# Kernel optimization log

Measured on AMD Instinct MI355X. Metric: run time of the kernel, lower is better.

## Reference

```python
import jax, jax.numpy as jnp
import numpy as np

B = 1024        # probe batch
Q = 65536       # queue_size (number of identities in momentum queue)
D = 512         # feat_dim
MARGIN = 0.4
SCALE = 32.0
HARD_NEG = 10   # min(max(int(Q*0.0002), 3), 10)


def setup_inputs() -> dict:
    key = jax.random.key(0)
    k1, k2, k3, k4 = jax.random.split(key, 4)
    p = jax.random.normal(k1, (B, D), dtype=jnp.float32)
    p = p / jnp.linalg.norm(p, axis=1, keepdims=True)
    queue = jax.random.uniform(k2, (2, Q, D), dtype=jnp.float32)
    queue = queue / jnp.linalg.norm(queue, axis=2, keepdims=True)  # F.normalize(queue, dim=2)
    label = jax.random.randint(k3, (B,), 0, Q)
    label = jnp.where(jnp.arange(B) % 4 == 0, -1, label)
    # binary mask buffer marking queue slots whose second copy is active
    mask = (jax.random.uniform(k4, (Q, 1)) < 0.1).astype(jnp.float32)
    return {"p": p, "queue": queue, "mask": mask, "label": label}


def _add_margin_am(cos_theta, label):
    # cos_theta: [B, Q], label: [B] with -1 marking outliers
    pos_mask = label != -1                                  # [B]
    safe_label = jnp.where(pos_mask, label, 0)
    onehot = jax.nn.one_hot(safe_label, cos_theta.shape[1], dtype=cos_theta.dtype)
    # AM-softmax: subtract margin at the ground-truth logit, then scale + CE
    logits = (cos_theta - MARGIN * onehot) * SCALE          # [B, Q]
    log_z = jax.nn.logsumexp(logits, axis=1)                # [B]
    gt = jnp.take_along_axis(cos_theta, safe_label[:, None], axis=1)[:, 0]
    ce = log_z - (gt - MARGIN) * SCALE                      # per-row cross entropy
    n_pos = jnp.sum(pos_mask)
    cls_loss = jnp.where(
        n_pos > 0,
        jnp.sum(jnp.where(pos_mask, ce, 0.0)) / jnp.maximum(n_pos, 1),
        0.0,
    )
    # hard-negative mining over outlier rows: top-k (replaces torch argsort+gather)
    top_vals, _ = jax.lax.top_k(cos_theta, HARD_NEG)        # [B, HARD_NEG]
    hard = jnp.clip(top_vals, 0.0)
    neg_per_row = jnp.mean(hard, axis=1)                    # [B]
    n_neg = jnp.sum(~pos_mask)
    neg_loss = jnp.where(
        n_neg > 0,
        jnp.sum(jnp.where(~pos_mask, neg_per_row, 0.0)) / jnp.maximum(n_neg, 1),
        0.0,
    )
    return cls_loss + neg_loss


def reference(p, queue, mask, label):
    # cos_theta1 = F.linear(p, queue[0])
    cos1 = jnp.einsum('bd,qd->bq', p, queue[0])
    # weight = mask * queue[1] + (1 - mask) * queue[0]  (computed under no_grad in torch)
    weight = mask * queue[1] + (1.0 - mask) * queue[0]
    cos2 = jnp.einsum('bd,qd->bq', p, weight)
    loss = _add_margin_am(cos1, label) + _add_margin_am(cos2, label)
    return loss
```

## Files before the change

### kernel.cpp

```cpp
#include <hip/hip_runtime.h>
#include <stdint.h>

#define B_ 1024
#define Q_ 65536
#define D_ 512
#define MT 128
#define NT 128
#define BK 64
#define NSPLIT 64
#define NCHUNK (Q_ / NSPLIT)
#define NTILES (NCHUNK / NT)
#define KITERS (D_ / BK)

#define SCALE32 32.0f
#define C32 46.16624130844683f

#define WS_ACC  0
#define WS_LSE  4096
#define WS_TOPK (1u * 1024u * 1024u)
#define WS_PBF  (8u * 1024u * 1024u)
#define WS_QBF0 (12u * 1024u * 1024u)
#define WS_WBF  (76u * 1024u * 1024u)

#define SA_OFF 0
#define SB0_OFF 16384
#define SB1_OFF 32768

typedef __attribute__((ext_vector_type(8))) short short8;
typedef __attribute__((ext_vector_type(4))) short short4v;
typedef __attribute__((ext_vector_type(4))) float f32x4;

__device__ __forceinline__ unsigned short f2bf(float x) {
  union { float f; uint32_t u; } v; v.f = x;
  uint32_t r = v.u + 0x7fffu + ((v.u >> 16) & 1u);
  return (unsigned short)(r >> 16);
}

__device__ __forceinline__ float bf2f(short u) {
  union { uint32_t i; float f; } v;
  v.i = ((uint32_t)(unsigned short)u) << 16;
  return v.f;
}

__device__ __forceinline__ void async16(void* lds, const void* g) {
  void* gg = (void*)g;
  __builtin_amdgcn_global_load_lds(
      (__attribute__((address_space(1))) unsigned int*)gg,
      (__attribute__((address_space(3))) unsigned int*)lds,
      16, 0, 0);
}

__device__ __forceinline__ void tkins(float v,
    float& t0, float& t1, float& t2, float& t3, float& t4,
    float& t5, float& t6, float& t7, float& t8, float& t9) {
  if (v > t9) {
    t9 = (v > t8) ? t8 : v;
    t8 = (v > t8) ? ((v > t7) ? t7 : v) : t8;
    t7 = (v > t7) ? ((v > t6) ? t6 : v) : t7;
    t6 = (v > t6) ? ((v > t5) ? t5 : v) : t6;
    t5 = (v > t5) ? ((v > t4) ? t4 : v) : t5;
    t4 = (v > t4) ? ((v > t3) ? t3 : v) : t4;
    t3 = (v > t3) ? ((v > t2) ? t2 : v) : t3;
    t2 = (v > t2) ? ((v > t1) ? t1 : v) : t2;
    t1 = (v > t1) ? ((v > t0) ? t0 : v) : t1;
    t0 = (v > t0) ? v : t0;
  }
}

#define TKA(v, a) tkins((v), a[0], a[1], a[2], a[3], a[4], a[5], a[6], a[7], a[8], a[9])

__global__ void cvt_all(const float* __restrict__ q, const float* __restrict__ p,
                        const float* __restrict__ mask,
                        unsigned short* __restrict__ qbf0,
                        unsigned short* __restrict__ wbf,
                        unsigned short* __restrict__ pbf) {
  const int wv = threadIdx.x >> 6;
  const int lane = threadIdx.x & 63;
  const int b = blockIdx.x;
  if (b < Q_ / 4) {
    const int row = b * 4 + wv;
    const float* q0r = q + (size_t)row * D_ + lane * 8;
    float4 a = ((const float4*)q0r)[0];
    float4 bb = ((const float4*)q0r)[1];
    short8 o;
    o[0] = (short)f2bf(a.x); o[1] = (short)f2bf(a.y);
    o[2] = (short)f2bf(a.z); o[3] = (short)f2bf(a.w);
    o[4] = (short)f2bf(bb.x); o[5] = (short)f2bf(bb.y);
    o[6] = (short)f2bf(bb.z); o[7] = (short)f2bf(bb.w);
    *(short8*)(qbf0 + (size_t)row * D_ + lane * 8) = o;
    float m = mask[row];
    if (m != 0.0f) {
      const float* q1r = q0r + (size_t)Q_ * D_;
      float4 c = ((const float4*)q1r)[0];
      float4 d = ((const float4*)q1r)[1];
      a.x = fmaf(m, c.x - a.x, a.x); a.y = fmaf(m, c.y - a.y, a.y);
      a.z = fmaf(m, c.z - a.z, a.z); a.w = fmaf(m, c.w - a.w, a.w);
      bb.x = fmaf(m, d.x - bb.x, bb.x); bb.y = fmaf(m, d.y - bb.y, bb.y);
      bb.z = fmaf(m, d.z - bb.z, bb.z); bb.w = fmaf(m, d.w - bb.w, bb.w);
      o[0] = (short)f2bf(a.x); o[1] = (short)f2bf(a.y);
      o[2] = (short)f2bf(a.z); o[3] = (short)f2bf(a.w);
      o[4] = (short)f2bf(bb.x); o[5] = (short)f2bf(bb.y);
      o[6] = (short)f2bf(bb.z); o[7] = (short)f2bf(bb.w);
      *(short8*)(wbf + (size_t)row * D_ + lane * 8) = o;
    }
  } else {
    const int row = (b - Q_ / 4) * 4 + wv;
    const float* pr = p + (size_t)row * D_ + lane * 8;
    float4 a = ((const float4*)pr)[0];
    float4 bb = ((const float4*)pr)[1];
    short8 o;
    o[0] = (short)f2bf(a.x); o[1] = (short)f2bf(a.y);
    o[2] = (short)f2bf(a.z); o[3] = (short)f2bf(a.w);
    o[4] = (short)f2bf(bb.x); o[5] = (short)f2bf(bb.y);
    o[6] = (short)f2bf(bb.z); o[7] = (short)f2bf(bb.w);
    *(short8*)(pbf + (size_t)row * D_ + lane * 8) = o;
  }
}

__global__ __launch_bounds__(256, 2) void fused_gemm_partial(
    const unsigned short* __restrict__ pbf,
    const unsigned short* __restrict__ qbf0,
    const unsigned short* __restrict__ wbf,
    const float* __restrict__ maskp,
    const int* __restrict__ label,
    char* __restrict__ ws) {
  __shared__ __align__(16) unsigned char smem[49152];
  __shared__ float maskb[NT];
  __shared__ float zacc[MT][4];
  __shared__ int olist[MT];
  __shared__ int rowmap[MT];
  __shared__ int sh_ocount;

  const int tid = threadIdx.x;
  const int split = blockIdx.x;
  const int mblk = blockIdx.y;
  const int lane = tid & 63;
  const int wv = tid >> 6;
  const int wr = wv >> 1;
  const int wc = wv & 1;
  const int lr = lane & 15;
  const int lg = lane >> 4;

  if (tid == 0) sh_ocount = 0;
  if (tid < MT) {
    rowmap[tid] = -1;
    zacc[tid][0] = 0.0f; zacc[tid][1] = 0.0f;
    zacc[tid][2] = 0.0f; zacc[tid][3] = 0.0f;
  }
  __syncthreads();
  if (tid < MT) {
    if (label[mblk * MT + tid] == -1) {
      int k = atomicAdd(&sh_ocount, 1);
      olist[k] = tid;
    }
  }
  __syncthreads();
  const int noc = sh_ocount;
  if (tid < noc) rowmap[olist[tid]] = tid;
  __syncthreads();
  const int nchunks = (noc + 31) >> 5;

  const int srow = lane >> 3;
  const int sc16 = (lane & 7) ^ srow;
  const size_t g_lane_off = (size_t)srow * D_ + sc16 * 8;

  float T[10];
#pragma unroll
  for (int i = 0; i < 10; ++i) T[i] = -1e30f;

  for (int nt = 0; nt < NTILES; ++nt) {
    const int nbase = split * NCHUNK + nt * NT;
    if (tid < NT) maskb[tid] = maskp[nbase + tid];
    __syncthreads();

    const unsigned short* b1b[4];
#pragma unroll
    for (int t = 0; t < 4; ++t) {
      const int rowl = (wv * 4 + t) * 8 + srow;
      b1b[t] = (maskb[rowl] != 0.0f) ? wbf : qbf0;
    }

    f32x4 acc0[4][4], acc1[4][4];
#pragma unroll
    for (int i = 0; i < 4; ++i)
#pragma unroll
      for (int j = 0; j < 4; ++j) {
        f32x4 z = {0.0f, 0.0f, 0.0f, 0.0f};
        acc0[i][j] = z;
        acc1[i][j] = z;
      }

    for (int kk = 0; kk < KITERS; ++kk) {
      const size_t kcol = (size_t)kk * BK;
#pragma unroll
      for (int t = 0; t < 4; ++t) {
        const int slot = wv * 4 + t;
        const size_t rbase = (size_t)slot * 8;
        async16(smem + SA_OFF + slot * 1024,
                pbf + ((size_t)mblk * MT + rbase) * D_ + kcol + g_lane_off);
        async16(smem + SB0_OFF + slot * 1024,
                qbf0 + ((size_t)nbase + rbase) * D_ + kcol + g_lane_off);
        async16(smem + SB1_OFF + slot * 1024,
                b1b[t] + ((size_t)nbase + rbase) * D_ + kcol + g_lane_off);
      }
      __syncthreads();

#pragma unroll
      for (int s = 0; s < 2; ++s) {
        const int xs = ((s * 4 + lg) ^ (lr & 7)) * 16;
        short8 af[4], bf[4];
#pragma unroll
        for (int i = 0; i < 4; ++i)
          af[i] = *(const short8*)(smem + SA_OFF + (wr * 64 + i * 16 + lr) * 128 + xs);
#pragma unroll
        for (int j = 0; j < 4; ++j)
          bf[j] = *(const short8*)(smem + SB0_OFF + (wc * 64 + j * 16 + lr) * 128 + xs);
#pragma unroll
        for (int i = 0; i < 4; ++i)
#pragma unroll
          for (int j = 0; j < 4; ++j)
            acc0[i][j] = __builtin_amdgcn_mfma_f32_16x16x32_bf16(af[i], bf[j], acc0[i][j], 0, 0, 0);
#pragma unroll
        for (int j = 0; j < 4; ++j)
          bf[j] = *(const short8*)(smem + SB1_OFF + (wc * 64 + j * 16 + lr) * 128 + xs);
#pragma unroll
        for (int i = 0; i < 4; ++i)
#pragma unroll
          for (int j = 0; j < 4; ++j)
            acc1[i][j] = __builtin_amdgcn_mfma_f32_16x16x32_bf16(af[i], bf[j], acc1[i][j], 0, 0, 0);
      }
      __syncthreads();
    }

#pragma unroll
    for (int i = 0; i < 4; ++i)
#pragma unroll
      for (int k = 0; k < 4; ++k) {
        float a0 = 0.0f, a1 = 0.0f;
#pragma unroll
        for (int j = 0; j < 4; ++j) {
          a0 += __builtin_amdgcn_exp2f(fmaf(acc0[i][j][k], C32, -C32));
          a1 += __builtin_amdgcn_exp2f(fmaf(acc1[i][j][k], C32, -C32));
        }
#pragma unroll
        for (int m = 1; m < 16; m <<= 1) {
          a0 += __shfl_xor(a0, m, 64);
          a1 += __shfl_xor(a1, m, 64);
        }
        if (lr == 0) {
          const int r = wr * 64 + i * 16 + lg * 4 + k;
          zacc[r][wc * 2 + 0] += a0;
          zacc[r][wc * 2 + 1] += a1;
        }
      }

    for (int c = 0; c < nchunks; ++c) {
      unsigned short* cp = (unsigned short*)smem;
#pragma unroll
      for (int i = 0; i < 4; ++i)
#pragma unroll
        for (int k = 0; k < 4; ++k) {
          const int r = wr * 64 + i * 16 + lg * 4 + k;
          const int o = rowmap[r];
          const int ol = o - c * 32;
          if (o >= 0 && ol >= 0 && ol < 32) {
#pragma unroll
            for (int j = 0; j < 4; ++j) {
              const int col = wc * 64 + j * 16 + lr;
              cp[ol * 128 + col] = f2bf(acc0[i][j][k]);
              cp[(32 + ol) * 128 + col] = f2bf(acc1[i][j][k]);
            }
          }
        }
      __syncthreads();

      {
        float tl[10];
#pragma unroll
        for (int r = 0; r < 10; ++r) tl[r] = -1e30f;
        const int pair = tid >> 2;
        const int q4 = tid & 3;
        const int orow = pair >> 1, mat = pair & 1;
        const int o = c * 32 + orow;
        if (o < noc) {
          const unsigned short* rp = cp + (mat * 32 + orow) * 128 + q4 * 32;
#pragma unroll
          for (int cc = 0; cc < 8; ++cc) {
            short4v v = *(const short4v*)(rp + cc * 4);
            TKA(bf2f(v.x), tl); TKA(bf2f(v.y), tl);
            TKA(bf2f(v.z), tl); TKA(bf2f(v.w), tl);
          }
          float ot[10];
#pragma unroll
          for (int r = 0; r < 10; ++r) ot[r] = __shfl_xor(tl[r], 1, 64);
#pragma unroll
          for (int r = 0; r < 10; ++r) TKA(ot[r], tl);
#pragma unroll
          for (int r = 0; r < 10; ++r) ot[r] = __shfl_xor(tl[r], 2, 64);
#pragma unroll
          for (int r = 0; r < 10; ++r) TKA(ot[r], tl);
          if (q4 == 0) {
            if (c == 0) {
#pragma unroll
              for (int r = 0; r < 10; ++r) TKA(tl[r], T);
            } else {
              float* slot = (float*)(ws + WS_TOPK) +
                  ((size_t)(mat * B_ + mblk * MT + olist[o]) * NSPLIT + split) * 10;
              if (nt == 0) {
#pragma unroll
                for (int r = 0; r < 10; ++r) slot[r] = tl[r];
              } else {
                float cur[10];
#pragma unroll
                for (int r = 0; r < 10; ++r) cur[r] = slot[r];
#pragma unroll
                for (int r = 0; r < 10; ++r) TKA(tl[r], cur);
#pragma unroll
                for (int r = 0; r < 10; ++r) slot[r] = cur[r];
              }
            }
          }
        }
      }
      __syncthreads();
    }
  }

  if (tid < MT) {
    float2* lseo = (float2*)(ws + WS_LSE);
    lseo[(size_t)(mblk * MT + tid) * NSPLIT + split] =
        make_float2(zacc[tid][0] + zacc[tid][2], zacc[tid][1] + zacc[tid][3]);
  }
  {
    const int pair = tid >> 2;
    const int q4 = tid & 3;
    const int orow = pair >> 1, mat = pair & 1;
    if (q4 == 0 && orow < noc && orow < 32) {
      float* slot = (float*)(ws + WS_TOPK) +
          ((size_t)(mat * B_ + mblk * MT + olist[orow]) * NSPLIT + split) * 10;
#pragma unroll
      for (int r = 0; r < 10; ++r) slot[r] = T[r];
    }
  }
}

__global__ void finalize_rows(
    const float* __restrict__ p, const float* __restrict__ queue,
    const float* __restrict__ maskp, const int* __restrict__ label,
    char* __restrict__ ws, float* __restrict__ out) {
  const int row = blockIdx.x;
  const int l = threadIdx.x >> 6;
  const int lane = threadIdx.x & 63;
  const int lab = label[row];
  float* wsf = (float*)ws;
  int* wsi = (int*)ws;

  if (lab != -1) {
    const float2* lsep = (const float2*)(ws + WS_LSE) + (size_t)row * NSPLIT;
    float2 zz = lsep[lane];
    float z = (l == 0) ? zz.x : zz.y;
#pragma unroll
    for (int o = 1; o < 64; o <<= 1) z += __shfl_xor(z, o, 64);

    const float* prow = p + (size_t)row * D_;
    const float* q0r = queue + (size_t)lab * D_;
    const float* q1r = queue + ((size_t)Q_ + (size_t)lab) * D_;
    int c = lane * 8;
    float4 a0 = *(const float4*)(prow + c);
    float4 a1 = *(const float4*)(prow + c + 4);
    float4 b0 = *(const float4*)(q0r + c);
    float4 b1 = *(const float4*)(q0r + c + 4);
    float d0 = a0.x * b0.x + a0.y * b0.y + a0.z * b0.z + a0.w * b0.w
             + a1.x * b1.x + a1.y * b1.y + a1.z * b1.z + a1.w * b1.w;
    float d1 = 0.0f;
    if (l == 1) {
      float4 c0 = *(const float4*)(q1r + c);
      float4 c1 = *(const float4*)(q1r + c + 4);
      d1 = a0.x * c0.x + a0.y * c0.y + a0.z * c0.z + a0.w * c0.w
         + a1.x * c1.x + a1.y * c1.y + a1.z * c1.z + a1.w * c1.w;
    }
#pragma unroll
    for (int o = 1; o < 64; o <<= 1) {
      d0 += __shfl_xor(d0, o, 64);
      d1 += __shfl_xor(d1, o, 64);
    }
    float gt;
    if (l == 0) gt = d0;
    else { float m = maskp[lab]; gt = fmaf(m, d1 - d0, d0); }

    if (lane == 0) {
      float e1 = __builtin_amdgcn_exp2f(fmaf(gt, C32, -C32));
      float e2 = __builtin_amdgcn_exp2f(fmaf(gt - 0.4f, C32, -C32));
      float Zc = z - e1 + e2;
      float ce = 32.0f + __logf(Zc) - (gt - 0.4f) * SCALE32;
      atomicAdd(&wsf[0], ce);
      if (l == 0) atomicAdd(&wsi[2], 1);
    }
  } else {
    const float* tp = (const float*)(ws + WS_TOPK) +
                      ((size_t)l * B_ + row) * NSPLIT * 10 + (size_t)lane * 10;
    float t0 = tp[0], t1 = tp[1], t2 = tp[2], t3 = tp[3], t4 = tp[4];
    float t5 = tp[5], t6 = tp[6], t7 = tp[7], t8 = tp[8], t9 = tp[9];
    float ssum = 0.0f;
#pragma unroll
    for (int r10 = 0; r10 < 10; ++r10) {
      float v = t0;
      int idx = lane;
#pragma unroll
      for (int o = 1; o < 64; o <<= 1) {
        float ov = __shfl_xor(v, o, 64);
        int oi = __shfl_xor(idx, o, 64);
        bool take = (ov > v) || (ov == v && oi < idx);
        v = take ? ov : v;
        idx = take ? oi : idx;
      }
      ssum += fmaxf(v, 0.0f);
      if (idx == lane) {
        t0 = t1; t1 = t2; t2 = t3; t3 = t4; t4 = t5;
        t5 = t6; t6 = t7; t7 = t8; t8 = t9; t9 = -1e30f;
      }
    }
    if (lane == 0) {
      atomicAdd(&wsf[1], ssum * 0.1f);
      if (l == 0) atomicAdd(&wsi[3], 1);
    }
  }

  __syncthreads();
  if (threadIdx.x == 0) {
    __threadfence();
    int old = atomicAdd(&wsi[4], 1);
    if (old == B_ - 1) {
      float ce = atomicAdd(&wsf[0], 0.0f);
      float ng = atomicAdd(&wsf[1], 0.0f);
      int np = atomicAdd(&wsi[2], 0);
      int nn = atomicAdd(&wsi[3], 0);
      float loss = 0.0f;
      if (np > 0) loss += ce / (float)np;
      if (nn > 0) loss += ng / (float)nn;
      out[0] = loss;
    }
  }
}

extern "C" void kernel_launch(void* const* d_in, const int* in_sizes, int n_in,
                              void* d_out, int out_size, void* d_ws, size_t ws_size,
                              hipStream_t stream) {
  const float* p     = (const float*)d_in[0];
  const float* queue = (const float*)d_in[1];
  const float* maskp = (const float*)d_in[2];
  const int*   label = (const int*)d_in[3];
  float* out = (float*)d_out;
  char* ws = (char*)d_ws;

  unsigned short* pbf  = (unsigned short*)(ws + WS_PBF);
  unsigned short* qbf0 = (unsigned short*)(ws + WS_QBF0);
  unsigned short* wbf  = (unsigned short*)(ws + WS_WBF);

  hipMemsetAsync(ws, 0, 32, stream);

  cvt_all<<<Q_ / 4 + B_ / 4, 256, 0, stream>>>(queue, p, maskp, qbf0, wbf, pbf);

  dim3 g1(NSPLIT, B_ / MT);
  fused_gemm_partial<<<g1, 256, 0, stream>>>(pbf, qbf0, wbf, maskp, label, ws);
  finalize_rows<<<B_, 128, 0, stream>>>(p, queue, maskp, label, ws, out);
}
```

Measured before the change: 598.0 us.

## Triple-buffer GEMM k-loop with async prefetch, widen to 8 waves, deterministic final reduce

The GEMM kernel moves from 256 to 512 threads (8 waves, each covering 32 columns) and replaces the load-sync-compute-sync k-loop with a 3-stage shared-memory ring. Global-to-LDS copies for k+2 are issued while k is computed, with vmcnt waits and one barrier per step. The end-of-loss atomics and the last-block counter are replaced by per-row writes plus a separate single-block reduce kernel, which removes the memset. LDS use grows to 144KB per block, which likely limits occupancy to one block per CU despite the launch bound.

Result: slower. 638.2 us (+6.7%).

```diff
diff --git a/kernel.cpp b/kernel.cpp
--- a/kernel.cpp
+++ b/kernel.cpp
@@ -15,13 +15,14 @@
 #define SCALE32 32.0f
 #define C32 46.16624130844683f
 
-#define WS_ACC  0
-#define WS_LSE  4096
+#define WS_ROWV 0
+#define WS_LSE  16384
 #define WS_TOPK (1u * 1024u * 1024u)
 #define WS_PBF  (8u * 1024u * 1024u)
 #define WS_QBF0 (12u * 1024u * 1024u)
 #define WS_WBF  (76u * 1024u * 1024u)
 
+#define SBUF 49152
 #define SA_OFF 0
 #define SB0_OFF 16384
 #define SB1_OFF 32768
@@ -117,16 +118,16 @@
   }
 }
 
-__global__ __launch_bounds__(256, 2) void fused_gemm_partial(
+__global__ __launch_bounds__(512, 2) void fused_gemm_partial(
     const unsigned short* __restrict__ pbf,
     const unsigned short* __restrict__ qbf0,
     const unsigned short* __restrict__ wbf,
     const float* __restrict__ maskp,
     const int* __restrict__ label,
     char* __restrict__ ws) {
-  __shared__ __align__(16) unsigned char smem[49152];
+  __shared__ __align__(16) unsigned char smem[3 * SBUF];
   __shared__ float maskb[NT];
-  __shared__ float zacc[MT][4];
+  __shared__ float zacc[MT][8];
   __shared__ int olist[MT];
   __shared__ int rowmap[MT];
   __shared__ int sh_ocount;
@@ -136,16 +137,16 @@
   const int mblk = blockIdx.y;
   const int lane = tid & 63;
   const int wv = tid >> 6;
-  const int wr = wv >> 1;
-  const int wc = wv & 1;
+  const int wr = wv >> 2;
+  const int wc = wv & 3;
   const int lr = lane & 15;
   const int lg = lane >> 4;
 
   if (tid == 0) sh_ocount = 0;
   if (tid < MT) {
     rowmap[tid] = -1;
-    zacc[tid][0] = 0.0f; zacc[tid][1] = 0.0f;
-    zacc[tid][2] = 0.0f; zacc[tid][3] = 0.0f;
+#pragma unroll
+    for (int c = 0; c < 8; ++c) zacc[tid][c] = 0.0f;
   }
   __syncthreads();
   if (tid < MT) {
@@ -173,63 +174,76 @@
     if (tid < NT) maskb[tid] = maskp[nbase + tid];
     __syncthreads();
 
-    const unsigned short* b1b[4];
-#pragma unroll
-    for (int t = 0; t < 4; ++t) {
-      const int rowl = (wv * 4 + t) * 8 + srow;
+    const unsigned short* b1b[2];
+#pragma unroll
+    for (int t = 0; t < 2; ++t) {
+      const int rowl = (wv * 2 + t) * 8 + srow;
       b1b[t] = (maskb[rowl] != 0.0f) ? wbf : qbf0;
     }
 
-    f32x4 acc0[4][4], acc1[4][4];
+    f32x4 acc0[4][2], acc1[4][2];
 #pragma unroll
     for (int i = 0; i < 4; ++i)
 #pragma unroll
-      for (int j = 0; j < 4; ++j) {
+      for (int j = 0; j < 2; ++j) {
         f32x4 z = {0.0f, 0.0f, 0.0f, 0.0f};
         acc0[i][j] = z;
         acc1[i][j] = z;
       }
 
+    auto stage = [&](int buf, int kk) {
+      const size_t kcol = (size_t)kk * BK;
+      unsigned char* sb = smem + (size_t)buf * SBUF;
+#pragma unroll
+      for (int t = 0; t < 2; ++t) {
+        const int slot = wv * 2 + t;
+        const size_t rbase = (size_t)slot * 8;
+        async16(sb + SA_OFF + slot * 1024,
+                pbf + ((size_t)mblk * MT + rbase) * D_ + kcol + g_lane_off);
+        async16(sb + SB0_OFF + slot * 1024,
+                qbf0 + ((size_t)nbase + rbase) * D_ + kcol + g_lane_off);
+        async16(sb + SB1_OFF + slot * 1024,
+                b1b[t] + ((size_t)nbase + rbase) * D_ + kcol + g_lane_off);
+      }
+    };
+
+    stage(0, 0);
+    stage(1, 1);
+
+#pragma unroll
     for (int kk = 0; kk < KITERS; ++kk) {
-      const size_t kcol = (size_t)kk * BK;
-#pragma unroll
-      for (int t = 0; t < 4; ++t) {
-        const int slot = wv * 4 + t;
-        const size_t rbase = (size_t)slot * 8;
-        async16(smem + SA_OFF + slot * 1024,
-                pbf + ((size_t)mblk * MT + rbase) * D_ + kcol + g_lane_off);
-        async16(smem + SB0_OFF + slot * 1024,
-                qbf0 + ((size_t)nbase + rbase) * D_ + kcol + g_lane_off);
-        async16(smem + SB1_OFF + slot * 1024,
-                b1b[t] + ((size_t)nbase + rbase) * D_ + kcol + g_lane_off);
-      }
-      __syncthreads();
-
+      if (kk < KITERS - 1)
+        asm volatile("s_waitcnt vmcnt(6)" ::: "memory");
+      else
+        asm volatile("s_waitcnt vmcnt(0)" ::: "memory");
+      __builtin_amdgcn_s_barrier();
+      if (kk < KITERS - 2) stage((kk + 2) % 3, kk + 2);
+
+      const unsigned char* sb = smem + (size_t)(kk % 3) * SBUF;
 #pragma unroll
       for (int s = 0; s < 2; ++s) {
         const int xs = ((s * 4 + lg) ^ (lr & 7)) * 16;
-        short8 af[4], bf[4];
+        short8 af[4], bf0[2], bf1[2];
 #pragma unroll
         for (int i = 0; i < 4; ++i)
-          af[i] = *(const short8*)(smem + SA_OFF + (wr * 64 + i * 16 + lr) * 128 + xs);
-#pragma unroll
-        for (int j = 0; j < 4; ++j)
-          bf[j] = *(const short8*)(smem + SB0_OFF + (wc * 64 + j * 16 + lr) * 128 + xs);
+          af[i] = *(const short8*)(sb + SA_OFF + (wr * 64 + i * 16 + lr) * 128 + xs);
+#pragma unroll
+        for (int j = 0; j < 2; ++j)
+          bf0[j] = *(const short8*)(sb + SB0_OFF + (wc * 32 + j * 16 + lr) * 128 + xs);
+#pragma unroll
+        for (int j = 0; j < 2; ++j)
+          bf1[j] = *(const short8*)(sb + SB1_OFF + (wc * 32 + j * 16 + lr) * 128 + xs);
 #pragma unroll
         for (int i = 0; i < 4; ++i)
 #pragma unroll
-          for (int j = 0; j < 4; ++j)
-            acc0[i][j] = __builtin_amdgcn_mfma_f32_16x16x32_bf16(af[i], bf[j], acc0[i][j], 0, 0, 0);
-#pragma unroll
-        for (int j = 0; j < 4; ++j)
-          bf[j] = *(const short8*)(smem + SB1_OFF + (wc * 64 + j * 16 + lr) * 128 + xs);
+          for (int j = 0; j < 2; ++j)
+            acc0[i][j] = __builtin_amdgcn_mfma_f32_16x16x32_bf16(af[i], bf0[j], acc0[i][j], 0, 0, 0);
 #pragma unroll
         for (int i = 0; i < 4; ++i)
 #pragma unroll
-          for (int j = 0; j < 4; ++j)
-            acc1[i][j] = __builtin_amdgcn_mfma_f32_16x16x32_bf16(af[i], bf[j], acc1[i][j], 0, 0, 0);
-      }
-      __syncthreads();
+          for (int j = 0; j < 2; ++j)
+            acc1[i][j] = __builtin_amdgcn_mfma_f32_16x16x32_bf16(af[i], bf1[j], acc1[i][j], 0, 0, 0);
+      }
     }
 
 #pragma unroll
@@ -238,7 +252,7 @@
       for (int k = 0; k < 4; ++k) {
         float a0 = 0.0f, a1 = 0.0f;
 #pragma unroll
-        for (int j = 0; j < 4; ++j) {
+        for (int j = 0; j < 2; ++j) {
           a0 += __builtin_amdgcn_exp2f(fmaf(acc0[i][j][k], C32, -C32));
           a1 += __builtin_amdgcn_exp2f(fmaf(acc1[i][j][k], C32, -C32));
         }
@@ -265,8 +279,8 @@
           const int ol = o - c * 32;
           if (o >= 0 && ol >= 0 && ol < 32) {
 #pragma unroll
-            for (int j = 0; j < 4; ++j) {
-              const int col = wc * 64 + j * 16 + lr;
+            for (int j = 0; j < 2; ++j) {
+              const int col = wc * 32 + j * 16 + lr;
               cp[ol * 128 + col] = f2bf(acc0[i][j][k]);
               cp[(32 + ol) * 128 + col] = f2bf(acc1[i][j][k]);
             }
@@ -282,7 +296,7 @@
         const int q4 = tid & 3;
         const int orow = pair >> 1, mat = pair & 1;
         const int o = c * 32 + orow;
-        if (o < noc) {
+        if (orow < 32 && o < noc) {
           const unsigned short* rp = cp + (mat * 32 + orow) * 128 + q4 * 32;
 #pragma unroll
           for (int cc = 0; cc < 8; ++cc) {
@@ -324,12 +338,15 @@
       }
       __syncthreads();
     }
-  }
-
+    if (nchunks > 1) asm volatile("s_waitcnt vmcnt(0)" ::: "memory");
+  }
+
+  __syncthreads();
   if (tid < MT) {
     float2* lseo = (float2*)(ws + WS_LSE);
-    lseo[(size_t)(mblk * MT + tid) * NSPLIT + split] =
-        make_float2(zacc[tid][0] + zacc[tid][2], zacc[tid][1] + zacc[tid][3]);
+    lseo[(size_t)(mblk * MT + tid) * NSPLIT + split] = make_float2(
+        zacc[tid][0] + zacc[tid][2] + zacc[tid][4] + zacc[tid][6],
+        zacc[tid][1] + zacc[tid][3] + zacc[tid][5] + zacc[tid][7]);
   }
   {
     const int pair = tid >> 2;
@@ -352,8 +369,7 @@
   const int l = threadIdx.x >> 6;
   const int lane = threadIdx.x & 63;
   const int lab = label[row];
-  float* wsf = (float*)ws;
-  int* wsi = (int*)ws;
+  float* rowv = (float*)(ws + WS_ROWV);
 
   if (lab != -1) {
     const float2* lsep = (const float2*)(ws + WS_LSE) + (size_t)row * NSPLIT;
@@ -393,8 +409,7 @@
       float e2 = __builtin_amdgcn_exp2f(fmaf(gt - 0.4f, C32, -C32));
       float Zc = z - e1 + e2;
       float ce = 32.0f + __logf(Zc) - (gt - 0.4f) * SCALE32;
-      atomicAdd(&wsf[0], ce);
-      if (l == 0) atomicAdd(&wsi[2], 1);
+      rowv[l * B_ + row] = ce;
     }
   } else {
     const float* tp = (const float*)(ws + WS_TOPK) +
@@ -420,26 +435,42 @@
         t5 = t6; t6 = t7; t7 = t8; t8 = t9; t9 = -1e30f;
       }
     }
-    if (lane == 0) {
-      atomicAdd(&wsf[1], ssum * 0.1f);
-      if (l == 0) atomicAdd(&wsi[3], 1);
-    }
-  }
-
+    if (lane == 0) rowv[l * B_ + row] = ssum * 0.1f;
+  }
+}
+
+__global__ void reduce_final(const int* __restrict__ label,
+                             const char* __restrict__ ws,
+                             float* __restrict__ out) {
+  __shared__ float sce[4], sng[4];
+  __shared__ int snp[4], snn[4];
+  const int tid = threadIdx.x;
+  const float* rowv = (const float*)(ws + WS_ROWV);
+  float ce = 0.0f, ng = 0.0f;
+  int np = 0, nn = 0;
+  for (int r = tid; r < B_; r += 256) {
+    float v = rowv[r] + rowv[B_ + r];
+    if (label[r] != -1) { ce += v; ++np; }
+    else { ng += v; ++nn; }
+  }
+#pragma unroll
+  for (int o = 1; o < 64; o <<= 1) {
+    ce += __shfl_xor(ce, o, 64);
+    ng += __shfl_xor(ng, o, 64);
+    np += __shfl_xor(np, o, 64);
+    nn += __shfl_xor(nn, o, 64);
+  }
+  const int wv = tid >> 6, lane = tid & 63;
+  if (lane == 0) { sce[wv] = ce; sng[wv] = ng; snp[wv] = np; snn[wv] = nn; }
   __syncthreads();
-  if (threadIdx.x == 0) {
-    __threadfence();
-    int old = atomicAdd(&wsi[4], 1);
-    if (old == B_ - 1) {
-      float ce = atomicAdd(&wsf[0], 0.0f);
-      float ng = atomicAdd(&wsf[1], 0.0f);
-      int np = atomicAdd(&wsi[2], 0);
-      int nn = atomicAdd(&wsi[3], 0);
-      float loss = 0.0f;
-      if (np > 0) loss += ce / (float)np;
-      if (nn > 0) loss += ng / (float)nn;
-      out[0] = loss;
-    }
+  if (tid == 0) {
+    float c = 0.0f, g = 0.0f; int p = 0, n = 0;
+#pragma unroll
+    for (int i = 0; i < 4; ++i) { c += sce[i]; g += sng[i]; p += snp[i]; n += snn[i]; }
+    float loss = 0.0f;
+    if (p > 0) loss += c / (float)p;
+    if (n > 0) loss += g / (float)n;
+    out[0] = loss;
   }
 }
 
@@ -457,11 +488,10 @@
   unsigned short* qbf0 = (unsigned short*)(ws + WS_QBF0);
   unsigned short* wbf  = (unsigned short*)(ws + WS_WBF);
 
-  hipMemsetAsync(ws, 0, 32, stream);
-
   cvt_all<<<Q_ / 4 + B_ / 4, 256, 0, stream>>>(queue, p, maskp, qbf0, wbf, pbf);
 
   dim3 g1(NSPLIT, B_ / MT);
-  fused_gemm_partial<<<g1, 256, 0, stream>>>(pbf, qbf0, wbf, maskp, label, ws);
+  fused_gemm_partial<<<g1, 512, 0, stream>>>(pbf, qbf0, wbf, maskp, label, ws);
   finalize_rows<<<B_, 128, 0, stream>>>(p, queue, maskp, label, ws, out);
-}
+  reduce_final<<<1, 256, 0, stream>>>(label, ws, out);
+}
```

## Compute second GEMM only on masked queue rows via compacted sparse correction

Applied to the files above, without the earlier changes.

Since weight equals queue[0] wherever mask is 0, the main GEMM now computes only p·queue[0]. A separate sparse GEMM runs over a compacted list of masked rows (built by a single-block scan) and adds the logsumexp correction and top-k candidates for cos2. This roughly halves MFMA work and B-operand traffic in the dense kernel, at the cost of a serial scan kernel, an extra gather GEMM launched over the maximum tile grid (most blocks exit early), and larger per-row merge work in finalize. The global atomics and last-block reduction are replaced by per-row outputs and a small final reduction kernel.

Result: slower. 689.9 us (+15.4%).

```diff
diff --git a/kernel.cpp b/kernel.cpp
--- a/kernel.cpp
+++ b/kernel.cpp
@@ -11,20 +11,21 @@
 #define NCHUNK (Q_ / NSPLIT)
 #define NTILES (NCHUNK / NT)
 #define KITERS (D_ / BK)
+#define MAXCT (Q_ / NT)
 
 #define SCALE32 32.0f
 #define C32 46.16624130844683f
 
-#define WS_ACC  0
-#define WS_LSE  4096
-#define WS_TOPK (1u * 1024u * 1024u)
-#define WS_PBF  (8u * 1024u * 1024u)
-#define WS_QBF0 (12u * 1024u * 1024u)
-#define WS_WBF  (76u * 1024u * 1024u)
-
-#define SA_OFF 0
-#define SB0_OFF 16384
-#define SB1_OFF 32768
+#define WS_ROWV  0u
+#define WS_META  16384u
+#define WS_MLIST 65536u
+#define WS_LSE   524288u
+#define WS_TOPK  (1u * 1024u * 1024u)
+#define WS_ZCORR (7u * 1024u * 1024u)
+#define WS_TOPKS (9u * 1024u * 1024u)
+#define WS_PBF   (30u * 1024u * 1024u)
+#define WS_QBF0  (32u * 1024u * 1024u)
+#define WS_WBF   (96u * 1024u * 1024u)
 
 typedef __attribute__((ext_vector_type(8))) short short8;
 typedef __attribute__((ext_vector_type(4))) short short4v;
@@ -68,6 +69,40 @@
 }
 
 #define TKA(v, a) tkins((v), a[0], a[1], a[2], a[3], a[4], a[5], a[6], a[7], a[8], a[9])
+
+__global__ __launch_bounds__(1024, 1) void compact_scan(
+    const float* __restrict__ mask, char* __restrict__ ws) {
+  __shared__ int wsum[16];
+  __shared__ int carry;
+  const int tid = threadIdx.x;
+  const int lane = tid & 63, wv = tid >> 6;
+  int* mlist = (int*)(ws + WS_MLIST);
+  if (tid == 0) carry = 0;
+  __syncthreads();
+  for (int c = 0; c < Q_ / 1024; ++c) {
+    const int r = c * 1024 + tid;
+    const bool m = mask[r] != 0.0f;
+    unsigned long long b = __ballot(m);
+    const int lpre = __popcll(b & ((1ull << lane) - 1ull));
+    if (lane == 0) wsum[wv] = __popcll(b);
+    __syncthreads();
+    int wbase = 0;
+#pragma unroll
+    for (int i = 0; i < 16; ++i) wbase += (i < wv) ? wsum[i] : 0;
+    int ctot = 0;
+#pragma unroll
+    for (int i = 0; i < 16; ++i) ctot += wsum[i];
+    if (m) mlist[carry + wbase + lpre] = r;
+    __syncthreads();
+    if (tid == 0) carry += ctot;
+    __syncthreads();
+  }
+  if (tid == 0) {
+    int* meta = (int*)(ws + WS_META);
+    meta[0] = carry;
+    meta[1] = (carry + NT - 1) / NT;
+  }
+}
 
 __global__ void cvt_all(const float* __restrict__ q, const float* __restrict__ p,
                         const float* __restrict__ mask,
@@ -120,13 +155,12 @@
 __global__ __launch_bounds__(256, 2) void fused_gemm_partial(
     const unsigned short* __restrict__ pbf,
     const unsigned short* __restrict__ qbf0,
-    const unsigned short* __restrict__ wbf,
     const float* __restrict__ maskp,
     const int* __restrict__ label,
     char* __restrict__ ws) {
-  __shared__ __align__(16) unsigned char smem[49152];
+  __shared__ __align__(16) unsigned char smem[32768];
   __shared__ float maskb[NT];
-  __shared__ float zacc[MT][4];
+  __shared__ float zacc[MT][2];
   __shared__ int olist[MT];
   __shared__ int rowmap[MT];
   __shared__ int sh_ocount;
@@ -142,11 +176,7 @@
   const int lg = lane >> 4;
 
   if (tid == 0) sh_ocount = 0;
-  if (tid < MT) {
-    rowmap[tid] = -1;
-    zacc[tid][0] = 0.0f; zacc[tid][1] = 0.0f;
-    zacc[tid][2] = 0.0f; zacc[tid][3] = 0.0f;
-  }
+  if (tid < MT) rowmap[tid] = -1;
   __syncthreads();
   if (tid < MT) {
     if (label[mblk * MT + tid] == -1) {
@@ -167,41 +197,42 @@
   float T[10];
 #pragma unroll
   for (int i = 0; i < 10; ++i) T[i] = -1e30f;
+  float zreg[4][4];
+#pragma unroll
+  for (int i = 0; i < 4; ++i)
+#pragma unroll
+    for (int k = 0; k < 4; ++k) zreg[i][k] = 0.0f;
 
   for (int nt = 0; nt < NTILES; ++nt) {
     const int nbase = split * NCHUNK + nt * NT;
     if (tid < NT) maskb[tid] = maskp[nbase + tid];
     __syncthreads();
 
-    const unsigned short* b1b[4];
-#pragma unroll
-    for (int t = 0; t < 4; ++t) {
-      const int rowl = (wv * 4 + t) * 8 + srow;
-      b1b[t] = (maskb[rowl] != 0.0f) ? wbf : qbf0;
-    }
-
-    f32x4 acc0[4][4], acc1[4][4];
+    f32x4 acc[4][4];
 #pragma unroll
     for (int i = 0; i < 4; ++i)
 #pragma unroll
       for (int j = 0; j < 4; ++j) {
         f32x4 z = {0.0f, 0.0f, 0.0f, 0.0f};
-        acc0[i][j] = z;
-        acc1[i][j] = z;
-      }
+        acc[i][j] = z;
+      }
+
+    const unsigned short* abase[4];
+    const unsigned short* bbase[4];
+#pragma unroll
+    for (int t = 0; t < 4; ++t) {
+      const int slot = wv * 4 + t;
+      abase[t] = pbf + ((size_t)mblk * MT + slot * 8) * D_ + g_lane_off;
+      bbase[t] = qbf0 + ((size_t)nbase + slot * 8) * D_ + g_lane_off;
+    }
 
     for (int kk = 0; kk < KITERS; ++kk) {
       const size_t kcol = (size_t)kk * BK;
 #pragma unroll
       for (int t = 0; t < 4; ++t) {
         const int slot = wv * 4 + t;
-        const size_t rbase = (size_t)slot * 8;
-        async16(smem + SA_OFF + slot * 1024,
-                pbf + ((size_t)mblk * MT + rbase) * D_ + kcol + g_lane_off);
-        async16(smem + SB0_OFF + slot * 1024,
-                qbf0 + ((size_t)nbase + rbase) * D_ + kcol + g_lane_off);
-        async16(smem + SB1_OFF + slot * 1024,
-                b1b[t] + ((size_t)nbase + rbase) * D_ + kcol + g_lane_off);
+        async16(smem + slot * 1024, abase[t] + kcol);
+        async16(smem + 16384 + slot * 1024, bbase[t] + kcol);
       }
       __syncthreads();
 
@@ -211,48 +242,33 @@
         short8 af[4], bf[4];
 #pragma unroll
         for (int i = 0; i < 4; ++i)
-          af[i] = *(const short8*)(smem + SA_OFF + (wr * 64 + i * 16 + lr) * 128 + xs);
+          af[i] = *(const short8*)(smem + (wr * 64 + i * 16 + lr) * 128 + xs);
 #pragma unroll
         for (int j = 0; j < 4; ++j)
-          bf[j] = *(const short8*)(smem + SB0_OFF + (wc * 64 + j * 16 + lr) * 128 + xs);
+          bf[j] = *(const short8*)(smem + 16384 + (wc * 64 + j * 16 + lr) * 128 + xs);
 #pragma unroll
         for (int i = 0; i < 4; ++i)
 #pragma unroll
           for (int j = 0; j < 4; ++j)
-            acc0[i][j] = __builtin_amdgcn_mfma_f32_16x16x32_bf16(af[i], bf[j], acc0[i][j], 0, 0, 0);
+            acc[i][j] = __builtin_amdgcn_mfma_f32_16x16x32_bf16(af[i], bf[j], acc[i][j], 0, 0, 0);
+      }
+      __syncthreads();
+    }
+
+#pragma unroll
+    for (int i = 0; i < 4; ++i)
+#pragma unroll
+      for (int k = 0; k < 4; ++k) {
+        float a0 = 0.0f;
 #pragma unroll
         for (int j = 0; j < 4; ++j)
-          bf[j] = *(const short8*)(smem + SB1_OFF + (wc * 64 + j * 16 + lr) * 128 + xs);
-#pragma unroll
-        for (int i = 0; i < 4; ++i)
-#pragma unroll
-          for (int j = 0; j < 4; ++j)
-            acc1[i][j] = __builtin_amdgcn_mfma_f32_16x16x32_bf16(af[i], bf[j], acc1[i][j], 0, 0, 0);
-      }
-      __syncthreads();
-    }
-
-#pragma unroll
-    for (int i = 0; i < 4; ++i)
-#pragma unroll
-      for (int k = 0; k < 4; ++k) {
-        float a0 = 0.0f, a1 = 0.0f;
-#pragma unroll
-        for (int j = 0; j < 4; ++j) {
-          a0 += __builtin_amdgcn_exp2f(fmaf(acc0[i][j][k], C32, -C32));
-          a1 += __builtin_amdgcn_exp2f(fmaf(acc1[i][j][k], C32, -C32));
-        }
-#pragma unroll
-        for (int m = 1; m < 16; m <<= 1) {
-          a0 += __shfl_xor(a0, m, 64);
-          a1 += __shfl_xor(a1, m, 64);
-        }
-        if (lr == 0) {
-          const int r = wr * 64 + i * 16 + lg * 4 + k;
-          zacc[r][wc * 2 + 0] += a0;
-          zacc[r][wc * 2 + 1] += a1;
-        }
-      }
+          a0 += __builtin_amdgcn_exp2f(fmaf(acc[i][j][k], C32, -C32));
+        zreg[i][k] += a0;
+      }
+
+    bool mflag[4];
+#pragma unroll
+    for (int j = 0; j < 4; ++j) mflag[j] = maskb[wc * 64 + j * 16 + lr] != 0.0f;
 
     for (int c = 0; c < nchunks; ++c) {
       unsigned short* cp = (unsigned short*)smem;
@@ -267,8 +283,9 @@
 #pragma unroll
             for (int j = 0; j < 4; ++j) {
               const int col = wc * 64 + j * 16 + lr;
-              cp[ol * 128 + col] = f2bf(acc0[i][j][k]);
-              cp[(32 + ol) * 128 + col] = f2bf(acc1[i][j][k]);
+              const unsigned short v = f2bf(acc[i][j][k]);
+              cp[ol * 128 + col] = v;
+              cp[(32 + ol) * 128 + col] = mflag[j] ? (unsigned short)0xFF80 : v;
             }
           }
         }
@@ -326,10 +343,19 @@
     }
   }
 
+#pragma unroll
+  for (int i = 0; i < 4; ++i)
+#pragma unroll
+    for (int k = 0; k < 4; ++k) {
+      float v = zreg[i][k];
+#pragma unroll
+      for (int m = 1; m < 16; m <<= 1) v += __shfl_xor(v, m, 64);
+      if (lr == 0) zacc[wr * 64 + i * 16 + lg * 4 + k][wc] = v;
+    }
+  __syncthreads();
   if (tid < MT) {
-    float2* lseo = (float2*)(ws + WS_LSE);
-    lseo[(size_t)(mblk * MT + tid) * NSPLIT + split] =
-        make_float2(zacc[tid][0] + zacc[tid][2], zacc[tid][1] + zacc[tid][3]);
+    ((float*)(ws + WS_LSE))[(size_t)(mblk * MT + tid) * NSPLIT + split] =
+        zacc[tid][0] + zacc[tid][1];
   }
   {
     const int pair = tid >> 2;
@@ -341,6 +367,195 @@
 #pragma unroll
       for (int r = 0; r < 10; ++r) slot[r] = T[r];
     }
+  }
+}
+
+__global__ __launch_bounds__(256, 2) void sparse_gemm(
+    const unsigned short* __restrict__ pbf,
+    const unsigned short* __restrict__ qbf0,
+    const unsigned short* __restrict__ wbf,
+    const int* __restrict__ label,
+    char* __restrict__ ws) {
+  const int* meta = (const int*)(ws + WS_META);
+  const int mcount = meta[0];
+  const int ct = blockIdx.x;
+  if (ct * NT >= mcount) return;
+  const int mblk = blockIdx.y;
+
+  __shared__ __align__(16) unsigned char smem[49152];
+  __shared__ int mrow[NT];
+  __shared__ float zsum[MT][2];
+  __shared__ int olist[MT];
+  __shared__ int rowmap[MT];
+  __shared__ int sh_ocount;
+
+  const int tid = threadIdx.x;
+  const int lane = tid & 63;
+  const int wv = tid >> 6;
+  const int wr = wv >> 1;
+  const int wc = wv & 1;
+  const int lr = lane & 15;
+  const int lg = lane >> 4;
+
+  if (tid == 0) sh_ocount = 0;
+  if (tid < MT) rowmap[tid] = -1;
+  if (tid < NT) {
+    const int ci = ct * NT + tid;
+    mrow[tid] = (ci < mcount) ? ((const int*)(ws + WS_MLIST))[ci] : -1;
+  }
+  __syncthreads();
+  if (tid < MT) {
+    if (label[mblk * MT + tid] == -1) {
+      int k = atomicAdd(&sh_ocount, 1);
+      olist[k] = tid;
+    }
+  }
+  __syncthreads();
+  const int noc = sh_ocount;
+  if (tid < noc) rowmap[olist[tid]] = tid;
+  __syncthreads();
+  const int nchunks = (noc + 31) >> 5;
+
+  const int srow = lane >> 3;
+  const int sc16 = (lane & 7) ^ srow;
+  const size_t g_lane_off = (size_t)srow * D_ + sc16 * 8;
+  const size_t c_lane_off = (size_t)sc16 * 8;
+
+  const unsigned short* abase[4];
+  size_t brow_off[4];
+#pragma unroll
+  for (int t = 0; t < 4; ++t) {
+    const int slot = wv * 4 + t;
+    abase[t] = pbf + ((size_t)mblk * MT + slot * 8) * D_ + g_lane_off;
+    int r = mrow[slot * 8 + srow];
+    brow_off[t] = (size_t)(r < 0 ? 0 : r) * D_ + c_lane_off;
+  }
+
+  f32x4 acc0[4][4], acc1[4][4];
+#pragma unroll
+  for (int i = 0; i < 4; ++i)
+#pragma unroll
+    for (int j = 0; j < 4; ++j) {
+      f32x4 z = {0.0f, 0.0f, 0.0f, 0.0f};
+      acc0[i][j] = z;
+      acc1[i][j] = z;
+    }
+
+  for (int kk = 0; kk < KITERS; ++kk) {
+    const size_t kcol = (size_t)kk * BK;
+#pragma unroll
+    for (int t = 0; t < 4; ++t) {
+      const int slot = wv * 4 + t;
+      async16(smem + slot * 1024, abase[t] + kcol);
+      async16(smem + 16384 + slot * 1024, qbf0 + brow_off[t] + kcol);
+      async16(smem + 32768 + slot * 1024, wbf + brow_off[t] + kcol);
+    }
+    __syncthreads();
+
+#pragma unroll
+    for (int s = 0; s < 2; ++s) {
+      const int xs = ((s * 4 + lg) ^ (lr & 7)) * 16;
+      short8 af[4], b0[4], b1[4];
+#pragma unroll
+      for (int i = 0; i < 4; ++i)
+        af[i] = *(const short8*)(smem + (wr * 64 + i * 16 + lr) * 128 + xs);
+#pragma unroll
+      for (int j = 0; j < 4; ++j)
+        b0[j] = *(const short8*)(smem + 16384 + (wc * 64 + j * 16 + lr) * 128 + xs);
+#pragma unroll
+      for (int j = 0; j < 4; ++j)
+        b1[j] = *(const short8*)(smem + 32768 + (wc * 64 + j * 16 + lr) * 128 + xs);
+#pragma unroll
+      for (int i = 0; i < 4; ++i)
+#pragma unroll
+        for (int j = 0; j < 4; ++j) {
+          acc0[i][j] = __builtin_amdgcn_mfma_f32_16x16x32_bf16(af[i], b0[j], acc0[i][j], 0, 0, 0);
+          acc1[i][j] = __builtin_amdgcn_mfma_f32_16x16x32_bf16(af[i], b1[j], acc1[i][j], 0, 0, 0);
+        }
+    }
+    __syncthreads();
+  }
+
+#pragma unroll
+  for (int i = 0; i < 4; ++i)
+#pragma unroll
+    for (int k = 0; k < 4; ++k) {
+      float d = 0.0f;
+#pragma unroll
+      for (int j = 0; j < 4; ++j) {
+        const int col = wc * 64 + j * 16 + lr;
+        const bool valid = (ct * NT + col) < mcount;
+        float e = __builtin_amdgcn_exp2f(fmaf(acc1[i][j][k], C32, -C32)) -
+                  __builtin_amdgcn_exp2f(fmaf(acc0[i][j][k], C32, -C32));
+        d += valid ? e : 0.0f;
+      }
+#pragma unroll
+      for (int m = 1; m < 16; m <<= 1) d += __shfl_xor(d, m, 64);
+      if (lr == 0) zsum[wr * 64 + i * 16 + lg * 4 + k][wc] = d;
+    }
+  __syncthreads();
+  if (tid < MT) {
+    ((float*)(ws + WS_ZCORR))[(size_t)(mblk * MT + tid) * MAXCT + ct] =
+        zsum[tid][0] + zsum[tid][1];
+  }
+
+  for (int c = 0; c < nchunks; ++c) {
+    unsigned short* cp = (unsigned short*)smem;
+#pragma unroll
+    for (int i = 0; i < 4; ++i)
+#pragma unroll
+      for (int k = 0; k < 4; ++k) {
+        const int r = wr * 64 + i * 16 + lg * 4 + k;
+        const int o = rowmap[r];
+        const int ol = o - c * 32;
+        if (o >= 0 && ol >= 0 && ol < 32) {
+#pragma unroll
+          for (int j = 0; j < 4; ++j) {
+            const int col = wc * 64 + j * 16 + lr;
+            const bool valid = (ct * NT + col) < mcount;
+            cp[ol * 128 + col] = valid ? f2bf(acc1[i][j][k]) : (unsigned short)0xFF80;
+          }
+        }
+      }
+    __syncthreads();
+
+    {
+      float tl[10];
+#pragma unroll
+      for (int r = 0; r < 10; ++r) tl[r] = -1e30f;
+      const int orow = tid >> 3;
+      const int q8 = tid & 7;
+      const int o = c * 32 + orow;
+      if (o < noc) {
+        const unsigned short* rp = cp + orow * 128 + q8 * 16;
+#pragma unroll
+        for (int cc = 0; cc < 4; ++cc) {
+          short4v v = *(const short4v*)(rp + cc * 4);
+          TKA(bf2f(v.x), tl); TKA(bf2f(v.y), tl);
+          TKA(bf2f(v.z), tl); TKA(bf2f(v.w), tl);
+        }
+        float ot[10];
+#pragma unroll
+        for (int r = 0; r < 10; ++r) ot[r] = __shfl_xor(tl[r], 1, 64);
+#pragma unroll
+        for (int r = 0; r < 10; ++r) TKA(ot[r], tl);
+#pragma unroll
+        for (int r = 0; r < 10; ++r) ot[r] = __shfl_xor(tl[r], 2, 64);
+#pragma unroll
+        for (int r = 0; r < 10; ++r) TKA(ot[r], tl);
+#pragma unroll
+        for (int r = 0; r < 10; ++r) ot[r] = __shfl_xor(tl[r], 4, 64);
+#pragma unroll
+        for (int r = 0; r < 10; ++r) TKA(ot[r], tl);
+        if (q8 == 0) {
+          float* slot = (float*)(ws + WS_TOPKS) +
+              ((size_t)(mblk * MT + olist[o]) * MAXCT + ct) * 10;
+#pragma unroll
+          for (int r = 0; r < 10; ++r) slot[r] = tl[r];
+        }
+      }
+    }
+    __syncthreads();
   }
 }
 
@@ -352,15 +567,22 @@
   const int l = threadIdx.x >> 6;
   const int lane = threadIdx.x & 63;
   const int lab = label[row];
-  float* wsf = (float*)ws;
-  int* wsi = (int*)ws;
+  float* rowv = (float*)(ws + WS_ROWV);
+  const int nct = ((const int*)(ws + WS_META))[1];
 
   if (lab != -1) {
-    const float2* lsep = (const float2*)(ws + WS_LSE) + (size_t)row * NSPLIT;
-    float2 zz = lsep[lane];
-    float z = (l == 0) ? zz.x : zz.y;
+    const float* lsep = (const float*)(ws + WS_LSE) + (size_t)row * NSPLIT;
+    float z = lsep[lane];
 #pragma unroll
     for (int o = 1; o < 64; o <<= 1) z += __shfl_xor(z, o, 64);
+    if (l == 1) {
+      const float* zcp = (const float*)(ws + WS_ZCORR) + (size_t)row * MAXCT;
+      float zc = 0.0f;
+      for (int t = lane; t < nct; t += 64) zc += zcp[t];
+#pragma unroll
+      for (int o = 1; o < 64; o <<= 1) zc += __shfl_xor(zc, o, 64);
+      z += zc;
+    }
 
     const float* prow = p + (size_t)row * D_;
     const float* q0r = queue + (size_t)lab * D_;
@@ -393,18 +615,26 @@
       float e2 = __builtin_amdgcn_exp2f(fmaf(gt - 0.4f, C32, -C32));
       float Zc = z - e1 + e2;
       float ce = 32.0f + __logf(Zc) - (gt - 0.4f) * SCALE32;
-      atomicAdd(&wsf[0], ce);
-      if (l == 0) atomicAdd(&wsi[2], 1);
+      rowv[l * B_ + row] = ce;
     }
   } else {
+    float tl[10];
     const float* tp = (const float*)(ws + WS_TOPK) +
                       ((size_t)l * B_ + row) * NSPLIT * 10 + (size_t)lane * 10;
-    float t0 = tp[0], t1 = tp[1], t2 = tp[2], t3 = tp[3], t4 = tp[4];
-    float t5 = tp[5], t6 = tp[6], t7 = tp[7], t8 = tp[8], t9 = tp[9];
+#pragma unroll
+    for (int r = 0; r < 10; ++r) tl[r] = tp[r];
+    if (l == 1) {
+      const float* sp = (const float*)(ws + WS_TOPKS) + (size_t)row * MAXCT * 10;
+      for (int t = lane; t < nct; t += 64) {
+        const float* spp = sp + (size_t)t * 10;
+#pragma unroll
+        for (int r = 0; r < 10; ++r) TKA(spp[r], tl);
+      }
+    }
     float ssum = 0.0f;
 #pragma unroll
     for (int r10 = 0; r10 < 10; ++r10) {
-      float v = t0;
+      float v = tl[0];
       int idx = lane;
 #pragma unroll
       for (int o = 1; o < 64; o <<= 1) {
@@ -416,30 +646,47 @@
       }
       ssum += fmaxf(v, 0.0f);
       if (idx == lane) {
-        t0 = t1; t1 = t2; t2 = t3; t3 = t4; t4 = t5;
-        t5 = t6; t6 = t7; t7 = t8; t8 = t9; t9 = -1e30f;
-      }
-    }
-    if (lane == 0) {
-      atomicAdd(&wsf[1], ssum * 0.1f);
-      if (l == 0) atomicAdd(&wsi[3], 1);
-    }
-  }
-
-  __syncthreads();
-  if (threadIdx.x == 0) {
-    __threadfence();
-    int old = atomicAdd(&wsi[4], 1);
-    if (old == B_ - 1) {
-      float ce = atomicAdd(&wsf[0], 0.0f);
-      float ng = atomicAdd(&wsf[1], 0.0f);
-      int np = atomicAdd(&wsi[2], 0);
-      int nn = atomicAdd(&wsi[3], 0);
-      float loss = 0.0f;
-      if (np > 0) loss += ce / (float)np;
-      if (nn > 0) loss += ng / (float)nn;
-      out[0] = loss;
-    }
+#pragma unroll
+        for (int q = 0; q < 9; ++q) tl[q] = tl[q + 1];
+        tl[9] = -1e30f;
+      }
+    }
+    if (lane == 0) rowv[l * B_ + row] = ssum * 0.1f;
+  }
+}
+
+__global__ void reduce_final(const int* __restrict__ label,
+                             const char* __restrict__ ws,
+                             float* __restrict__ out) {
+  __shared__ float sce[4], sng[4];
+  __shared__ int snp[4], snn[4];
+  const int tid = threadIdx.x;
+  const float* rowv = (const float*)(ws + WS_ROWV);
+  float ce = 0.0f, ng = 0.0f;
+  int np = 0, nn = 0;
+  for (int r = tid; r < B_; r += 256) {
+    float v = rowv[r] + rowv[B_ + r];
+    if (label[r] != -1) { ce += v; ++np; }
+    else { ng += v; ++nn; }
+  }
+#pragma unroll
+  for (int o = 1; o < 64; o <<= 1) {
+    ce += __shfl_xor(ce, o, 64);
+    ng += __shfl_xor(ng, o, 64);
+    np += __shfl_xor(np, o, 64);
+    nn += __shfl_xor(nn, o, 64);
+  }
+  const int wv = tid >> 6, lane = tid & 63;
+  if (lane == 0) { sce[wv] = ce; sng[wv] = ng; snp[wv] = np; snn[wv] = nn; }
+  __syncthreads();
+  if (tid == 0) {
+    float c = 0.0f, g = 0.0f; int pp = 0, n = 0;
+#pragma unroll
+    for (int i = 0; i < 4; ++i) { c += sce[i]; g += sng[i]; pp += snp[i]; n += snn[i]; }
+    float loss = 0.0f;
+    if (pp > 0) loss += c / (float)pp;
+    if (n > 0) loss += g / (float)n;
+    out[0] = loss;
   }
 }
 
@@ -457,11 +704,15 @@
   unsigned short* qbf0 = (unsigned short*)(ws + WS_QBF0);
   unsigned short* wbf  = (unsigned short*)(ws + WS_WBF);
 
-  hipMemsetAsync(ws, 0, 32, stream);
-
+  compact_scan<<<1, 1024, 0, stream>>>(maskp, ws);
   cvt_all<<<Q_ / 4 + B_ / 4, 256, 0, stream>>>(queue, p, maskp, qbf0, wbf, pbf);
 
   dim3 g1(NSPLIT, B_ / MT);
-  fused_gemm_partial<<<g1, 256, 0, stream>>>(pbf, qbf0, wbf, maskp, label, ws);
+  fused_gemm_partial<<<g1, 256, 0, stream>>>(pbf, qbf0, maskp, label, ws);
+
+  dim3 g2(MAXCT, B_ / MT);
+  sparse_gemm<<<g2, 256, 0, stream>>>(pbf, qbf0, wbf, label, ws);
+
   finalize_rows<<<B_, 128, 0, stream>>>(p, queue, maskp, label, ws, out);
-}
+  reduce_final<<<1, 256, 0, stream>>>(label, ws, out);
+}
```
